# Performance work log

Hardware: AMD Instinct MI355X
Metric: run time of the kernel (lower is better)

Reference implementation:

```python
import jax, jax.numpy as jnp
import numpy as np

DIM = 192
HEADS = 6
HIDDEN = 384  # int(DIM * 2.0)


def _ln(x, w, b):
    # WithBias LayerNorm over channel dim (torch normalizes last dim of b,(hw),c)
    mu = jnp.mean(x, axis=1, keepdims=True)
    var = jnp.var(x, axis=1, keepdims=True)
    return (x - mu) / jnp.sqrt(var + 1e-5) * w[None, :, None, None] + b[None, :, None, None]


def _conv1x1(x, w):  # w: [O, I, 1, 1]
    return jnp.einsum('bihw,oi->bohw', x, w[:, :, 0, 0])


def _dwconv3(x, w):  # depthwise 3x3, w: [C, 1, 3, 3]
    return jax.lax.conv_general_dilated(
        x, w, window_strides=(1, 1), padding=((1, 1), (1, 1)),
        feature_group_count=x.shape[1],
        dimension_numbers=('NCHW', 'OIHW', 'NCHW'))


def _l2norm(x):  # F.normalize along last axis
    n = jnp.sqrt(jnp.sum(x * x, axis=-1, keepdims=True))
    return x / jnp.maximum(n, 1e-12)


def setup_inputs() -> dict:
    key = jax.random.key(0)
    ks = jax.random.split(key, 16)
    s = 0.02
    d = {}
    d['x'] = jax.random.normal(ks[0], (2, DIM, 128, 128), dtype=jnp.float32)
    d['k_v'] = jax.random.normal(ks[1], (2, 256), dtype=jnp.float32)
    d['ln1_w'] = jnp.ones((DIM,), jnp.float32)
    d['ln1_b'] = jnp.zeros((DIM,), jnp.float32)
    d['temp'] = jnp.ones((HEADS, 1, 1), jnp.float32)
    d['w_kR'] = jax.random.normal(ks[2], (DIM * 3 // 4, 192), jnp.float32) * s
    d['w_kI'] = jax.random.normal(ks[3], (DIM // 4, 64), jnp.float32) * s
    d['w_qR'] = jax.random.normal(ks[4], (DIM, DIM * 3 // 4, 1, 1), jnp.float32) * s
    d['w_qdw'] = jax.random.normal(ks[5], (DIM, 1, 3, 3), jnp.float32) * s
    d['w_kvI'] = jax.random.normal(ks[6], (DIM * 2, DIM // 4, 1, 1), jnp.float32) * s
    d['w_kvdw'] = jax.random.normal(ks[7], (DIM * 2, 1, 3, 3), jnp.float32) * s
    d['w_po'] = jax.random.normal(ks[8], (DIM, DIM, 1, 1), jnp.float32) * s
    d['ln2_w'] = jnp.ones((DIM,), jnp.float32)
    d['ln2_b'] = jnp.zeros((DIM,), jnp.float32)
    d['w_ffk'] = jax.random.normal(ks[9], (DIM, 256), jnp.float32) * s
    d['w_pin'] = jax.random.normal(ks[10], (HIDDEN * 2, DIM, 1, 1), jnp.float32) * s
    d['w_dw'] = jax.random.normal(ks[11], (HIDDEN * 2, 1, 3, 3), jnp.float32) * s
    d['w_pout'] = jax.random.normal(ks[12], (DIM, HIDDEN, 1, 1), jnp.float32) * s
    return d


def reference(x, k_v, ln1_w, ln1_b, temp, w_kR, w_kI, w_qR, w_qdw, w_kvI, w_kvdw,
              w_po, ln2_w, ln2_b, w_ffk, w_pin, w_dw, w_pout):
    b, c, h, w = x.shape
    c3 = c * 3 // 4
    # ---- Rttention on norm1(x) ----
    xn = _ln(x, ln1_w, ln1_b)
    kvr = (k_v[:, :192] @ w_kR.T)[:, :, None, None]   # [b, 3c/4, 1, 1]
    kvi = (k_v[:, 192:] @ w_kI.T)[:, :, None, None]   # [b, c/4, 1, 1]
    x_r = xn[:, :c3] * kvr + xn[:, :c3]
    x_i = xn[:, c3:] * kvi + xn[:, c3:]
    q = _dwconv3(_conv1x1(x_r, w_qR), w_qdw)          # [b, c, h, w]
    kv = _dwconv3(_conv1x1(x_i, w_kvI), w_kvdw)       # [b, 2c, h, w]
    k, v = jnp.split(kv, 2, axis=1)
    rh = lambda t: t.reshape(b, HEADS, c // HEADS, h * w)
    q = _l2norm(rh(q))
    k = _l2norm(rh(k))
    v = rh(v)
    # channel-wise attention: [b, head, c_h, c_h]
    attn = jax.nn.softmax(jnp.einsum('bhcd,bhed->bhce', q, k) * temp[None], axis=-1)
    out = jnp.einsum('bhce,bhed->bhcd', attn, v).reshape(b, c, h, w)
    x = x + _conv1x1(out, w_po)
    # ---- GDFN FeedForward on norm2(x) ----
    xn2 = _ln(x, ln2_w, ln2_b)
    kvf = (k_v @ w_ffk.T)[:, :, None, None]           # [b, c, 1, 1]
    y = xn2 * kvf + xn2
    y = _dwconv3(_conv1x1(y, w_pin), w_dw)            # [b, 2*hidden, h, w]
    y1, y2 = jnp.split(y, 2, axis=1)
    y = jax.nn.gelu(y1, approximate=False) * y2
    x = x + _conv1x1(y, w_pout)
    return (x, k_v)
```

## Files before the change

### kernel.cpp

```cpp
#include <hip/hip_runtime.h>
#include <math.h>

#define HW 16384
#define IMG 128
#define CDIM 192
#define C3 144
#define C4 48
#define NB 2
#define NPX 32768
#define HEADS 6

typedef unsigned short u16;
typedef unsigned int u32;
typedef __attribute__((ext_vector_type(8))) short bf16x8;
typedef __attribute__((ext_vector_type(4))) float f32x4;

__device__ __forceinline__ float bf2f(u16 u) {
    return __uint_as_float(((unsigned int)u) << 16);
}
__device__ __forceinline__ u16 f2bf(float f) {
    unsigned int x = __float_as_uint(f);
    unsigned int r = x + 0x7fffu + ((x >> 16) & 1u);
    return (u16)(r >> 16);
}

static inline float* wsf(void* ws, size_t off) { return (float*)((char*)ws + off); }
static inline u16* wsh(void* ws, size_t off) { return (u16*)((char*)ws + off); }

__global__ void k_setup(const float* __restrict__ kvv, const float* __restrict__ wkR,
                        const float* __restrict__ wkI, const float* __restrict__ wffk,
                        const float* __restrict__ wqR, const float* __restrict__ wkvI,
                        const float* __restrict__ wpo, const float* __restrict__ wpin,
                        const float* __restrict__ wpout,
                        u16* __restrict__ wb, float* __restrict__ sm,
                        float* __restrict__ tail) {
    int t = blockIdx.x * 256 + threadIdx.x;
    if (t < 313344) {
        float v;
        if (t < 30720) {
            int o = t / 160, i = t % 160;
            v = (i < 144) ? wqR[o * 144 + i] : 0.f;
        } else if (t < 55296) {
            int r = t - 30720; int o = r / 64, i = r % 64;
            v = (i < 48) ? wkvI[o * 48 + i] : 0.f;
        } else if (t < 92160) {
            v = wpo[t - 55296];
        } else if (t < 239616) {
            v = wpin[t - 92160];
        } else {
            v = wpout[t - 239616];
        }
        wb[t] = f2bf(v);
    } else if (t < 314112) {
        int r = t - 313344;
        if (r < 288) {
            int b = r / 144, o = r % 144;
            const float* v = kvv + b * 256;
            const float* w = wkR + o * 192;
            float s = 0.f;
            for (int j = 0; j < 192; j++) s += v[j] * w[j];
            sm[r] = s + 1.0f;
        } else if (r < 384) {
            int r2 = r - 288;
            int b = r2 / 48, o = r2 % 48;
            const float* v = kvv + b * 256 + 192;
            const float* w = wkI + o * 64;
            float s = 0.f;
            for (int j = 0; j < 64; j++) s += v[j] * w[j];
            sm[288 + r2] = s + 1.0f;
        } else {
            int r2 = r - 384;
            int b = r2 / 192, o = r2 % 192;
            const float* v = kvv + b * 256;
            const float* w = wffk + o * 256;
            float s = 0.f;
            for (int j = 0; j < 256; j++) s += v[j] * w[j];
            sm[384 + r2] = s + 1.0f;
        }
    } else if (t < 314624) {
        int r = t - 314112;
        tail[r] = kvv[r];
    } else if (t < 326912) {
        sm[3840 + (t - 314624)] = 0.f;
    }
}

__global__ void k_setup2(const float* __restrict__ wpin, const float* __restrict__ lnw,
                         const float* __restrict__ lnb, const float* __restrict__ kvf,
                         u16* __restrict__ wpinb, float* __restrict__ rsum,
                         float* __restrict__ biasp) {
    int t = blockIdx.x * 256 + threadIdx.x;
    if (t >= 1536) return;
    int b = t / 768, m = t % 768;
    float rs = 0.f, bi = 0.f;
    u16* wrow = wpinb + (size_t)t * 192;
    for (int c = 0; c < 192; c++) {
        float w = wpin[m * 192 + c];
        float s = kvf[b * 192 + c];
        u16 h = f2bf(w * lnw[c] * s);
        wrow[c] = h;
        rs += bf2f(h);
        bi += w * lnb[c] * s;
    }
    rsum[t] = rs;
    biasp[t] = bi;
}

__global__ __launch_bounds__(256) void k_ln1(
    const float* __restrict__ x,
    const float* __restrict__ lnw, const float* __restrict__ lnb,
    const float* __restrict__ sca, const float* __restrict__ scb,
    u16* __restrict__ outA, u16* __restrict__ outB, u16* __restrict__ xb16) {
    __shared__ float red[2][16][16][4];
    __shared__ float mu_s[16][4], rstd_s[16][4];
    int t = threadIdx.x;
    int px4 = t & 15, cg = t >> 4;
    int base = blockIdx.x * 64;
    int b = base >> 14;
    int p = (base & 16383) + px4 * 4;
    float vals[12][4];
    float s[4] = {0.f, 0.f, 0.f, 0.f}, s2[4] = {0.f, 0.f, 0.f, 0.f};
#pragma unroll
    for (int j = 0; j < 12; j++) {
        int c = cg * 12 + j;
        size_t off = ((size_t)(b * CDIM + c)) * HW + p;
        float4 f = *(const float4*)(x + off);
        float v[4] = {f.x, f.y, f.z, f.w};
        ushort4 o;
        o.x = f2bf(v[0]); o.y = f2bf(v[1]); o.z = f2bf(v[2]); o.w = f2bf(v[3]);
        *(ushort4*)(xb16 + off) = o;
#pragma unroll
        for (int q = 0; q < 4; q++) { vals[j][q] = v[q]; s[q] += v[q]; s2[q] += v[q] * v[q]; }
    }
#pragma unroll
    for (int q = 0; q < 4; q++) { red[0][cg][px4][q] = s[q]; red[1][cg][px4][q] = s2[q]; }
    __syncthreads();
    if (t < 16) {
        float S[4] = {0.f, 0.f, 0.f, 0.f}, S2[4] = {0.f, 0.f, 0.f, 0.f};
        for (int g2 = 0; g2 < 16; g2++)
#pragma unroll
            for (int q = 0; q < 4; q++) { S[q] += red[0][g2][t][q]; S2[q] += red[1][g2][t][q]; }
#pragma unroll
        for (int q = 0; q < 4; q++) {
            float mu = S[q] * (1.0f / CDIM);
            float var = S2[q] * (1.0f / CDIM) - mu * mu;
            mu_s[t][q] = mu;
            rstd_s[t][q] = rsqrtf(var + 1e-5f);
        }
    }
    __syncthreads();
    float mu[4], rs[4];
#pragma unroll
    for (int q = 0; q < 4; q++) { mu[q] = mu_s[px4][q]; rs[q] = rstd_s[px4][q]; }
#pragma unroll
    for (int j = 0; j < 12; j++) {
        int c = cg * 12 + j;
        float w = lnw[c], bb = lnb[c];
        float sc; u16* op; size_t off;
        if (c < C3) { sc = sca[b * C3 + c]; off = ((size_t)(b * C3 + c)) * HW + p; op = outA; }
        else { sc = scb[b * C4 + c - C3]; off = ((size_t)(b * C4 + c - C3)) * HW + p; op = outB; }
        ushort4 o;
        o.x = f2bf(((vals[j][0] - mu[0]) * rs[0] * w + bb) * sc);
        o.y = f2bf(((vals[j][1] - mu[1]) * rs[1] * w + bb) * sc);
        o.z = f2bf(((vals[j][2] - mu[2]) * rs[2] * w + bb) * sc);
        o.w = f2bf(((vals[j][3] - mu[3]) * rs[3] * w + bb) * sc);
        *(ushort4*)(op + off) = o;
    }
}

__global__ __launch_bounds__(256) void k_gemm_qkv(
    const u16* __restrict__ Xq, const u16* __restrict__ Xkv,
    const u16* __restrict__ Wq, const u16* __restrict__ Wkv,
    u16* __restrict__ Oq, u16* __restrict__ Okv) {
    __shared__ __align__(16) u16 Ws[64 * 32];
    __shared__ __align__(16) u16 Xs[32 * 130];
    const int tid = threadIdx.x;
    const int n0 = blockIdx.x * 128;
    const int y = blockIdx.y;
    const int b = blockIdx.z;
    const u16* X; const u16* Wb; u16* Op; int nch, cip, xrows, CO, m0;
    if (y < 3) { X = Xq; Wb = Wq; Op = Oq; nch = 5; cip = 160; xrows = 144; CO = 192; m0 = y * 64; }
    else { X = Xkv; Wb = Wkv; Op = Okv; nch = 2; cip = 64; xrows = 48; CO = 384; m0 = (y - 3) * 64; }
    const u16* Xb = X + (size_t)b * xrows * HW + n0;
    const int wave = tid >> 6, lane = tid & 63;
    const int quad = lane >> 4, l16 = lane & 15;
    const int smr = tid >> 2, sk4 = tid & 3;
    const int skr = tid >> 3, sc0 = (tid & 7) * 16;
    f32x4 acc[4][2] = {};
    for (int ch = 0; ch < nch; ch++) {
        const int k0 = ch * 32;
        if (ch) __syncthreads();
        {
            const int4 wv = *(const int4*)(Wb + (size_t)(m0 + smr) * cip + k0 + sk4 * 8);
            *(int4*)&Ws[(smr << 5) + (((sk4 ^ (smr & 3)) & 3) << 3)] = wv;
        }
        {
            const u16* xc = Xb + (size_t)(k0 + skr) * HW + sc0;
            int4 r0 = *(const int4*)xc;
            int4 r1 = *(const int4*)(xc + 8);
            u32* dst = (u32*)&Xs[skr * 130 + sc0];
#pragma unroll
            for (int i = 0; i < 4; i++) dst[i] = ((const u32*)&r0)[i];
#pragma unroll
            for (int i = 0; i < 4; i++) dst[4 + i] = ((const u32*)&r1)[i];
        }
        __syncthreads();
        bf16x8 af[4];
#pragma unroll
        for (int mi = 0; mi < 4; mi++) {
            int row = mi * 16 + l16;
            af[mi] = *(const bf16x8*)&Ws[(row << 5) + ((quad ^ (row & 3)) << 3)];
        }
#pragma unroll
        for (int ni = 0; ni < 2; ni++) {
            int n = wave * 32 + ni * 16 + l16;
            bf16x8 bfr;
#pragma unroll
            for (int j = 0; j < 8; j++) bfr[j] = (short)Xs[(quad * 8 + j) * 130 + n];
#pragma unroll
            for (int mi = 0; mi < 4; mi++)
                acc[mi][ni] = __builtin_amdgcn_mfma_f32_16x16x32_bf16(af[mi], bfr, acc[mi][ni], 0, 0, 0);
        }
    }
#pragma unroll
    for (int mi = 0; mi < 4; mi++)
#pragma unroll
        for (int ni = 0; ni < 2; ni++)
#pragma unroll
            for (int r = 0; r < 4; r++) {
                int m = m0 + mi * 16 + quad * 4 + r;
                int n = n0 + wave * 32 + ni * 16 + l16;
                Op[((size_t)b * CO + m) * HW + n] = f2bf(acc[mi][ni][r]);
            }
}

__global__ __launch_bounds__(256) void k_dw2m(const u16* __restrict__ Xq,
                                              const u16* __restrict__ Xkv,
                                              const float* __restrict__ Wdq,
                                              const float* __restrict__ Wdkv,
                                              u16* __restrict__ outq, u16* __restrict__ outkv,
                                              float* __restrict__ sqq, float* __restrict__ sqk) {
    __shared__ float In[34 * 132];
    __shared__ float red[4];
    int bid = blockIdx.x;
    const u16* X; const float* Wd; u16* out; float* sqp; int C;
    if (bid < 1536) { X = Xq; Wd = Wdq; out = outq; sqp = sqq; C = 192; }
    else { bid -= 1536; X = Xkv; Wd = Wdkv; out = outkv; sqp = sqk; C = 384; }
    int bc = bid >> 2, rt = bid & 3;
    int b = bc / C, ch = bc % C;
    const u16* xb = X + (size_t)bc * HW;
    int t = threadIdx.x;
    int c0 = (t & 7) * 16;
    for (int r = t >> 3; r < 34; r += 32) {
        int y = rt * 32 - 1 + r;
        float* dst = &In[r * 132 + 1 + c0];
        if ((unsigned)y < 128u) {
            const u16* src = xb + y * 128 + c0;
            int4 r0 = *(const int4*)src;
            int4 r1 = *(const int4*)(src + 8);
            const u16* p0 = (const u16*)&r0;
            const u16* p1 = (const u16*)&r1;
#pragma unroll
            for (int i = 0; i < 8; i++) dst[i] = bf2f(p0[i]);
#pragma unroll
            for (int i = 0; i < 8; i++) dst[8 + i] = bf2f(p1[i]);
        } else {
#pragma unroll
            for (int i = 0; i < 16; i++) dst[i] = 0.f;
        }
    }
    if (t < 34) { In[t * 132] = 0.f; In[t * 132 + 129] = 0.f; }
    __syncthreads();
    const float* w = Wd + ch * 9;
    float w00 = w[0], w01 = w[1], w02 = w[2], w10 = w[3], w11 = w[4],
          w12 = w[5], w20 = w[6], w21 = w[7], w22 = w[8];
    int x = t & 127, rg = t >> 7;
    int base = rg * 16;
    float A2 = 0.f, A1 = 0.f, B1 = 0.f, ssq = 0.f;
    u16* ob = out + (size_t)bc * HW + (rt * 32 + base) * 128 + x;
#pragma unroll
    for (int r = 0; r < 18; r++) {
        const float* row = &In[(base + r) * 132 + x];
        float v0 = row[0], v1 = row[1], v2 = row[2];
        float h0 = w00 * v0 + w01 * v1 + w02 * v2;
        float h1 = w10 * v0 + w11 * v1 + w12 * v2;
        float h2 = w20 * v0 + w21 * v1 + w22 * v2;
        if (r >= 2) {
            float val = A2 + B1 + h2;
            ob[(size_t)(r - 2) * 128] = f2bf(val);
            ssq += val * val;
        }
        A2 = A1; A1 = h0; B1 = h1;
    }
    if (ch < 192) {
        for (int o = 32; o > 0; o >>= 1) ssq += __shfl_down(ssq, o, 64);
        int wid = t >> 6, lane = t & 63;
        if (lane == 0) red[wid] = ssq;
        __syncthreads();
        if (t == 0) sqp[((b * 192 + ch) << 2) | rt] = red[0] + red[1] + red[2] + red[3];
    }
}

__global__ __launch_bounds__(256) void k_qk(const u16* __restrict__ qb_,
                                            const u16* __restrict__ kb_,
                                            float* __restrict__ S) {
    int bh = blockIdx.x >> 5, ds = blockIdx.x & 31;
    int b = bh / HEADS, h = bh % HEADS;
    int tid = threadIdx.x;
    int wave = tid >> 6, lane = tid & 63;
    int quad = lane >> 4, l16 = lane & 15;
    int tm = wave >> 1, tn = wave & 1;
    const u16* qrow = qb_ + ((size_t)(b * 192 + h * 32 + tm * 16 + l16)) * HW + ds * 512 + quad * 8;
    const u16* krow = kb_ + ((size_t)(b * 384 + h * 32 + tn * 16 + l16)) * HW + ds * 512 + quad * 8;
    f32x4 acc = {};
#pragma unroll
    for (int ch = 0; ch < 16; ch++) {
        bf16x8 a = *(const bf16x8*)(qrow + ch * 32);
        bf16x8 k8 = *(const bf16x8*)(krow + ch * 32);
        acc = __builtin_amdgcn_mfma_f32_16x16x32_bf16(a, k8, acc, 0, 0, 0);
    }
    float* Sb = S + bh * 1024;
#pragma unroll
    for (int r = 0; r < 4; r++)
        atomicAdd(&Sb[(tm * 16 + quad * 4 + r) * 32 + tn * 16 + l16], acc[r]);
}

__global__ __launch_bounds__(256) void k_smA(const float* __restrict__ S,
                                             const float* __restrict__ sqqp,
                                             const float* __restrict__ sqkp,
                                             const float* __restrict__ temp,
                                             const float* __restrict__ wpo,
                                             u16* __restrict__ weff) {
    __shared__ float A[32][33];
    __shared__ float scq[32], sck[32];
    int bh = blockIdx.x;
    int b = bh / HEADS, h = bh % HEADS;
    int t = threadIdx.x;
    if (t < 32) {
        const float* qp = sqqp + (b * 192 + h * 32 + t) * 4;
        const float* kp = sqkp + (b * 192 + h * 32 + t) * 4;
        scq[t] = 1.0f / fmaxf(sqrtf(qp[0] + qp[1] + qp[2] + qp[3]), 1e-12f);
        sck[t] = 1.0f / fmaxf(sqrtf(kp[0] + kp[1] + kp[2] + kp[3]), 1e-12f);
    }
    __syncthreads();
    float tmp = temp[h];
    for (int idx = t; idx < 1024; idx += 256) {
        int r = idx >> 5, e = idx & 31;
        A[r][e] = S[bh * 1024 + r * 32 + e] * scq[r] * sck[e] * tmp;
    }
    __syncthreads();
    if (t < 32) {
        float m = -1e30f;
        for (int e = 0; e < 32; e++) m = fmaxf(m, A[t][e]);
        float s = 0.f;
        for (int e = 0; e < 32; e++) { float ev = expf(A[t][e] - m); A[t][e] = ev; s += ev; }
        float inv = 1.0f / s;
        for (int e = 0; e < 32; e++) A[t][e] *= inv;
    }
    __syncthreads();
    for (int idx = t; idx < 6144; idx += 256) {
        int m = idx >> 5, e = idx & 31;
        float s = 0.f;
        const float* wr = wpo + m * 192 + h * 32;
#pragma unroll 8
        for (int c = 0; c < 32; c++) s += wr[c] * A[c][e];
        weff[((size_t)b * 192 + m) * 192 + h * 32 + e] = f2bf(s);
    }
}

__global__ __launch_bounds__(256) void k_gemm_po(
    const u16* __restrict__ kvb, const u16* __restrict__ weff,
    const u16* __restrict__ residb, u16* __restrict__ x1b,
    float* __restrict__ sumP, float* __restrict__ sum2P) {
    __shared__ __align__(16) u16 Ws[64 * 32];
    __shared__ __align__(16) u16 Xs[32 * 130];
    const int tid = threadIdx.x;
    const int n0 = blockIdx.x * 128;
    const int m0 = blockIdx.y * 64;
    const int b = blockIdx.z;
    const u16* Xb = kvb + ((size_t)b * 384 + 192) * HW + n0;
    const u16* Wb = weff + (size_t)b * 192 * 192;
    const int wave = tid >> 6, lane = tid & 63;
    const int quad = lane >> 4, l16 = lane & 15;
    const int smr = tid >> 2, sk4 = tid & 3;
    const int skr = tid >> 3, sc0 = (tid & 7) * 16;
    f32x4 acc[4][2] = {};
    for (int ch = 0; ch < 6; ch++) {
        const int k0 = ch * 32;
        if (ch) __syncthreads();
        {
            const int4 wv = *(const int4*)(Wb + (size_t)(m0 + smr) * 192 + k0 + sk4 * 8);
            *(int4*)&Ws[(smr << 5) + (((sk4 ^ (smr & 3)) & 3) << 3)] = wv;
        }
        {
            const u16* xc = Xb + (size_t)(k0 + skr) * HW + sc0;
            int4 r0 = *(const int4*)xc;
            int4 r1 = *(const int4*)(xc + 8);
            u32* dst = (u32*)&Xs[skr * 130 + sc0];
#pragma unroll
            for (int i = 0; i < 4; i++) dst[i] = ((const u32*)&r0)[i];
#pragma unroll
            for (int i = 0; i < 4; i++) dst[4 + i] = ((const u32*)&r1)[i];
        }
        __syncthreads();
        bf16x8 af[4];
#pragma unroll
        for (int mi = 0; mi < 4; mi++) {
            int row = mi * 16 + l16;
            af[mi] = *(const bf16x8*)&Ws[(row << 5) + ((quad ^ (row & 3)) << 3)];
        }
#pragma unroll
        for (int ni = 0; ni < 2; ni++) {
            int n = wave * 32 + ni * 16 + l16;
            bf16x8 bfr;
#pragma unroll
            for (int j = 0; j < 8; j++) bfr[j] = (short)Xs[(quad * 8 + j) * 130 + n];
#pragma unroll
            for (int mi = 0; mi < 4; mi++)
                acc[mi][ni] = __builtin_amdgcn_mfma_f32_16x16x32_bf16(af[mi], bfr, acc[mi][ni], 0, 0, 0);
        }
    }
#pragma unroll
    for (int ni = 0; ni < 2; ni++) {
        int nl = wave * 32 + ni * 16 + l16;
        float s1 = 0.f, s2 = 0.f;
#pragma unroll
        for (int mi = 0; mi < 4; mi++)
#pragma unroll
            for (int r = 0; r < 4; r++) {
                int m = m0 + mi * 16 + quad * 4 + r;
                size_t idx = ((size_t)(b * 192 + m)) * HW + n0 + nl;
                float v = acc[mi][ni][r] + bf2f(residb[idx]);
                s1 += v; s2 += v * v;
                x1b[idx] = f2bf(v);
            }
        s1 += __shfl_xor(s1, 16, 64); s1 += __shfl_xor(s1, 32, 64);
        s2 += __shfl_xor(s2, 16, 64); s2 += __shfl_xor(s2, 32, 64);
        if (quad == 0) {
            sumP[((size_t)(b * 3 + blockIdx.y)) * HW + n0 + nl] = s1;
            sum2P[((size_t)(b * 3 + blockIdx.y)) * HW + n0 + nl] = s2;
        }
    }
}

__global__ __launch_bounds__(256) void k_pin(
    const u16* __restrict__ X, const u16* __restrict__ wpb,
    const float* __restrict__ rsum, const float* __restrict__ biasp,
    const float* __restrict__ sumP, const float* __restrict__ sum2P,
    u16* __restrict__ out) {
    __shared__ __align__(16) u16 Ws[64 * 32];
    __shared__ __align__(16) u16 Xs[32 * 130];
    const int tid = threadIdx.x;
    const int n0 = blockIdx.x * 128;
    const int m0 = blockIdx.y * 64;
    const int b = blockIdx.z;
    const u16* Xb = X + (size_t)b * 192 * HW + n0;
    const u16* Wb = wpb + (size_t)b * 768 * 192;
    const int wave = tid >> 6, lane = tid & 63;
    const int quad = lane >> 4, l16 = lane & 15;
    const int smr = tid >> 2, sk4 = tid & 3;
    const int skr = tid >> 3, sc0 = (tid & 7) * 16;
    f32x4 acc[4][2] = {};
    for (int ch = 0; ch < 6; ch++) {
        const int k0 = ch * 32;
        if (ch) __syncthreads();
        {
            const int4 wv = *(const int4*)(Wb + (size_t)(m0 + smr) * 192 + k0 + sk4 * 8);
            *(int4*)&Ws[(smr << 5) + (((sk4 ^ (smr & 3)) & 3) << 3)] = wv;
        }
        {
            const u16* xc = Xb + (size_t)(k0 + skr) * HW + sc0;
            int4 r0 = *(const int4*)xc;
            int4 r1 = *(const int4*)(xc + 8);
            u32* dst = (u32*)&Xs[skr * 130 + sc0];
#pragma unroll
            for (int i = 0; i < 4; i++) dst[i] = ((const u32*)&r0)[i];
#pragma unroll
            for (int i = 0; i < 4; i++) dst[4 + i] = ((const u32*)&r1)[i];
        }
        __syncthreads();
        bf16x8 af[4];
#pragma unroll
        for (int mi = 0; mi < 4; mi++) {
            int row = mi * 16 + l16;
            af[mi] = *(const bf16x8*)&Ws[(row << 5) + ((quad ^ (row & 3)) << 3)];
        }
#pragma unroll
        for (int ni = 0; ni < 2; ni++) {
            int n = wave * 32 + ni * 16 + l16;
            bf16x8 bfr;
#pragma unroll
            for (int j = 0; j < 8; j++) bfr[j] = (short)Xs[(quad * 8 + j) * 130 + n];
#pragma unroll
            for (int mi = 0; mi < 4; mi++)
                acc[mi][ni] = __builtin_amdgcn_mfma_f32_16x16x32_bf16(af[mi], bfr, acc[mi][ni], 0, 0, 0);
        }
    }
    float rsv[4][4], biv[4][4];
#pragma unroll
    for (int mi = 0; mi < 4; mi++)
#pragma unroll
        for (int r = 0; r < 4; r++) {
            int m = m0 + mi * 16 + quad * 4 + r;
            rsv[mi][r] = rsum[b * 768 + m];
            biv[mi][r] = biasp[b * 768 + m];
        }
#pragma unroll
    for (int ni = 0; ni < 2; ni++) {
        int n = n0 + wave * 32 + ni * 16 + l16;
        size_t sb = (size_t)b * 3 * HW + n;
        float P = sumP[sb] + sumP[sb + HW] + sumP[sb + 2 * HW];
        float Q = sum2P[sb] + sum2P[sb + HW] + sum2P[sb + 2 * HW];
        float mu = P * (1.0f / 192.0f);
        float var = Q * (1.0f / 192.0f) - mu * mu;
        float rstd = rsqrtf(var + 1e-5f);
#pragma unroll
        for (int mi = 0; mi < 4; mi++)
#pragma unroll
            for (int r = 0; r < 4; r++) {
                int m = m0 + mi * 16 + quad * 4 + r;
                float v = rstd * (acc[mi][ni][r] - mu * rsv[mi][r]) + biv[mi][r];
                out[((size_t)(b * 768 + m)) * HW + n] = f2bf(v);
            }
    }
}

__global__ __launch_bounds__(256) void k_dw_gelu2(const u16* __restrict__ G0,
                                                  const float* __restrict__ Wd,
                                                  u16* __restrict__ out) {
    __shared__ float In[2 * 34 * 132];
    int bc = blockIdx.x >> 2, rt = blockIdx.x & 3;
    int b = bc / 384, j = bc % 384;
    int t = threadIdx.x;
    int c0 = (t & 7) * 16;
    for (int pl = 0; pl < 2; pl++) {
        const u16* xb = G0 + ((size_t)b * 768 + pl * 384 + j) * HW;
        float* pla = &In[pl * 34 * 132];
        for (int r = t >> 3; r < 34; r += 32) {
            int y = rt * 32 - 1 + r;
            float* dst = &pla[r * 132 + 1 + c0];
            if ((unsigned)y < 128u) {
                const u16* src = xb + y * 128 + c0;
                int4 r0 = *(const int4*)src;
                int4 r1 = *(const int4*)(src + 8);
                const u16* p0 = (const u16*)&r0;
                const u16* p1 = (const u16*)&r1;
#pragma unroll
                for (int i = 0; i < 8; i++) dst[i] = bf2f(p0[i]);
#pragma unroll
                for (int i = 0; i < 8; i++) dst[8 + i] = bf2f(p1[i]);
            } else {
#pragma unroll
                for (int i = 0; i < 16; i++) dst[i] = 0.f;
            }
        }
        if (t < 34) { pla[t * 132] = 0.f; pla[t * 132 + 129] = 0.f; }
    }
    __syncthreads();
    const float* w1 = Wd + j * 9;
    const float* w2 = Wd + (384 + j) * 9;
    float a00 = w1[0], a01 = w1[1], a02 = w1[2], a10 = w1[3], a11 = w1[4],
          a12 = w1[5], a20 = w1[6], a21 = w1[7], a22 = w1[8];
    float b00 = w2[0], b01 = w2[1], b02 = w2[2], b10 = w2[3], b11 = w2[4],
          b12 = w2[5], b20 = w2[6], b21 = w2[7], b22 = w2[8];
    int x = t & 127, rg = t >> 7;
    int base = rg * 16;
    float A2a = 0.f, A1a = 0.f, B1a = 0.f;
    float A2b = 0.f, A1b = 0.f, B1b = 0.f;
    u16* ob = out + ((size_t)b * 384 + j) * HW + (rt * 32 + base) * 128 + x;
#pragma unroll
    for (int r = 0; r < 18; r++) {
        const float* r1p = &In[(base + r) * 132 + x];
        const float* r2p = r1p + 34 * 132;
        float u0 = r1p[0], u1 = r1p[1], u2 = r1p[2];
        float v0 = r2p[0], v1 = r2p[1], v2 = r2p[2];
        float h0a = a00 * u0 + a01 * u1 + a02 * u2;
        float h1a = a10 * u0 + a11 * u1 + a12 * u2;
        float h2a = a20 * u0 + a21 * u1 + a22 * u2;
        float h0b = b00 * v0 + b01 * v1 + b02 * v2;
        float h1b = b10 * v0 + b11 * v1 + b12 * v2;
        float h2b = b20 * v0 + b21 * v1 + b22 * v2;
        if (r >= 2) {
            float s1 = A2a + B1a + h2a;
            float s2 = A2b + B1b + h2b;
            float g = 0.5f * s1 * (1.0f + erff(s1 * 0.70710678118654752f));
            ob[(size_t)(r - 2) * 128] = f2bf(g * s2);
        }
        A2a = A1a; A1a = h0a; B1a = h1a;
        A2b = A1b; A1b = h0b; B1b = h1b;
    }
}

__global__ __launch_bounds__(256) void k_gemm_pout(
    const u16* __restrict__ X, const u16* __restrict__ Wb,
    const u16* __restrict__ residb, float* __restrict__ out) {
    __shared__ __align__(16) u16 Ws[64 * 32];
    __shared__ __align__(16) u16 Xs[32 * 130];
    const int tid = threadIdx.x;
    const int n0 = blockIdx.x * 128;
    const int m0 = blockIdx.y * 64;
    const int b = blockIdx.z;
    const u16* Xb = X + (size_t)b * 384 * HW + n0;
    const int wave = tid >> 6, lane = tid & 63;
    const int quad = lane >> 4, l16 = lane & 15;
    const int smr = tid >> 2, sk4 = tid & 3;
    const int skr = tid >> 3, sc0 = (tid & 7) * 16;
    f32x4 acc[4][2] = {};
    for (int ch = 0; ch < 12; ch++) {
        const int k0 = ch * 32;
        if (ch) __syncthreads();
        {
            const int4 wv = *(const int4*)(Wb + (size_t)(m0 + smr) * 384 + k0 + sk4 * 8);
            *(int4*)&Ws[(smr << 5) + (((sk4 ^ (smr & 3)) & 3) << 3)] = wv;
        }
        {
            const u16* xc = Xb + (size_t)(k0 + skr) * HW + sc0;
            int4 r0 = *(const int4*)xc;
            int4 r1 = *(const int4*)(xc + 8);
            u32* dst = (u32*)&Xs[skr * 130 + sc0];
#pragma unroll
            for (int i = 0; i < 4; i++) dst[i] = ((const u32*)&r0)[i];
#pragma unroll
            for (int i = 0; i < 4; i++) dst[4 + i] = ((const u32*)&r1)[i];
        }
        __syncthreads();
        bf16x8 af[4];
#pragma unroll
        for (int mi = 0; mi < 4; mi++) {
            int row = mi * 16 + l16;
            af[mi] = *(const bf16x8*)&Ws[(row << 5) + ((quad ^ (row & 3)) << 3)];
        }
#pragma unroll
        for (int ni = 0; ni < 2; ni++) {
            int n = wave * 32 + ni * 16 + l16;
            bf16x8 bfr;
#pragma unroll
            for (int j = 0; j < 8; j++) bfr[j] = (short)Xs[(quad * 8 + j) * 130 + n];
#pragma unroll
            for (int mi = 0; mi < 4; mi++)
                acc[mi][ni] = __builtin_amdgcn_mfma_f32_16x16x32_bf16(af[mi], bfr, acc[mi][ni], 0, 0, 0);
        }
    }
#pragma unroll
    for (int mi = 0; mi < 4; mi++)
#pragma unroll
        for (int ni = 0; ni < 2; ni++)
#pragma unroll
            for (int r = 0; r < 4; r++) {
                int m = m0 + mi * 16 + quad * 4 + r;
                int n = n0 + wave * 32 + ni * 16 + l16;
                size_t idx = ((size_t)(b * 192 + m)) * HW + n;
                out[idx] = acc[mi][ni][r] + bf2f(residb[idx]);
            }
}

extern "C" void kernel_launch(void* const* d_in, const int* in_sizes, int n_in,
                              void* d_out, int out_size, void* d_ws, size_t ws_size,
                              hipStream_t stream) {
    const float* x     = (const float*)d_in[0];
    const float* k_v   = (const float*)d_in[1];
    const float* ln1w  = (const float*)d_in[2];
    const float* ln1b  = (const float*)d_in[3];
    const float* temp  = (const float*)d_in[4];
    const float* w_kR  = (const float*)d_in[5];
    const float* w_kI  = (const float*)d_in[6];
    const float* w_qR  = (const float*)d_in[7];
    const float* w_qdw = (const float*)d_in[8];
    const float* w_kvI = (const float*)d_in[9];
    const float* w_kvdw= (const float*)d_in[10];
    const float* w_po  = (const float*)d_in[11];
    const float* ln2w  = (const float*)d_in[12];
    const float* ln2b  = (const float*)d_in[13];
    const float* w_ffk = (const float*)d_in[14];
    const float* w_pin = (const float*)d_in[15];
    const float* w_dw  = (const float*)d_in[16];
    const float* w_pout= (const float*)d_in[17];
    float* out = (float*)d_out;

    const size_t MiB = 1048576ULL;
    u16*   xrb     = wsh(d_ws, 0);
    u16*   xib     = wsh(d_ws, 10 * MiB);
    u16*   xb16    = wsh(d_ws, 14 * MiB);
    u16*   q0b     = wsh(d_ws, 26 * MiB);
    u16*   kv0b    = wsh(d_ws, 38 * MiB);
    u16*   qbuf_b  = wsh(d_ws, 62 * MiB);
    u16*   kvbuf_b = wsh(d_ws, 74 * MiB);
    u16*   x1b     = wsh(d_ws, 98 * MiB);
    u16*   g0b     = wsh(d_ws, 110 * MiB);
    u16*   ybufb   = wsh(d_ws, 158 * MiB);
    u16*   wb      = wsh(d_ws, 182 * MiB);
    u16*   weffb   = wsh(d_ws, 183 * MiB);
    u16*   wpinb   = wsh(d_ws, 184 * MiB);
    float* sm      = wsf(d_ws, 185 * MiB);
    float* sumP    = wsf(d_ws, 186 * MiB);
    float* sum2P   = wsf(d_ws, 187 * MiB);
    u16* wq   = wb;
    u16* wkv  = wb + 30720;
    u16* wpout= wb + 239616;
    float* kvr  = sm;
    float* kvi  = sm + 288;
    float* kvf  = sm + 384;
    float* sqqp = sm + 768;
    float* sqkp = sm + 2304;
    float* Smat = sm + 3840;
    float* rsum = sm + 16128;
    float* biasp= sm + 17664;

    k_setup<<<1277, 256, 0, stream>>>(k_v, w_kR, w_kI, w_ffk, w_qR, w_kvI, w_po,
                                      w_pin, w_pout, wb, sm,
                                      out + (size_t)NB * CDIM * HW);
    k_setup2<<<6, 256, 0, stream>>>(w_pin, ln2w, ln2b, kvf, wpinb, rsum, biasp);
    k_ln1<<<NPX / 64, 256, 0, stream>>>(x, ln1w, ln1b, kvr, kvi, xrb, xib, xb16);
    k_gemm_qkv<<<dim3(128, 9, 2), 256, 0, stream>>>(xrb, xib, wq, wkv, q0b, kv0b);
    k_dw2m<<<4608, 256, 0, stream>>>(q0b, kv0b, w_qdw, w_kvdw, qbuf_b, kvbuf_b, sqqp, sqkp);
    k_qk<<<12 * 32, 256, 0, stream>>>(qbuf_b, kvbuf_b, Smat);
    k_smA<<<12, 256, 0, stream>>>(Smat, sqqp, sqkp, temp, w_po, weffb);
    k_gemm_po<<<dim3(128, 3, 2), 256, 0, stream>>>(kvbuf_b, weffb, xb16, x1b, sumP, sum2P);
    k_pin<<<dim3(128, 12, 2), 256, 0, stream>>>(x1b, wpinb, rsum, biasp, sumP, sum2P, g0b);
    k_dw_gelu2<<<NB * 384 * 4, 256, 0, stream>>>(g0b, w_dw, ybufb);
    k_gemm_pout<<<dim3(128, 3, 2), 256, 0, stream>>>(ybufb, wpout, x1b, out);
}
```

Before: 280.6 us.

## Merge setup kernels and keep depthwise conv halos in bf16 shared memory

```diff
diff --git a/kernel.cpp b/kernel.cpp
--- a/kernel.cpp
+++ b/kernel.cpp
@@ -30,80 +30,83 @@
 __global__ void k_setup(const float* __restrict__ kvv, const float* __restrict__ wkR,
                         const float* __restrict__ wkI, const float* __restrict__ wffk,
                         const float* __restrict__ wqR, const float* __restrict__ wkvI,
-                        const float* __restrict__ wpo, const float* __restrict__ wpin,
-                        const float* __restrict__ wpout,
+                        const float* __restrict__ wpout_f, const float* __restrict__ wpin,
+                        const float* __restrict__ ln2w, const float* __restrict__ ln2b,
                         u16* __restrict__ wb, float* __restrict__ sm,
-                        float* __restrict__ tail) {
-    int t = blockIdx.x * 256 + threadIdx.x;
-    if (t < 313344) {
-        float v;
-        if (t < 30720) {
-            int o = t / 160, i = t % 160;
-            v = (i < 144) ? wqR[o * 144 + i] : 0.f;
-        } else if (t < 55296) {
-            int r = t - 30720; int o = r / 64, i = r % 64;
-            v = (i < 48) ? wkvI[o * 48 + i] : 0.f;
-        } else if (t < 92160) {
-            v = wpo[t - 55296];
-        } else if (t < 239616) {
-            v = wpin[t - 92160];
-        } else {
-            v = wpout[t - 239616];
-        }
-        wb[t] = f2bf(v);
-    } else if (t < 314112) {
-        int r = t - 313344;
-        if (r < 288) {
-            int b = r / 144, o = r % 144;
-            const float* v = kvv + b * 256;
-            const float* w = wkR + o * 192;
-            float s = 0.f;
-            for (int j = 0; j < 192; j++) s += v[j] * w[j];
-            sm[r] = s + 1.0f;
-        } else if (r < 384) {
-            int r2 = r - 288;
-            int b = r2 / 48, o = r2 % 48;
-            const float* v = kvv + b * 256 + 192;
-            const float* w = wkI + o * 64;
-            float s = 0.f;
-            for (int j = 0; j < 64; j++) s += v[j] * w[j];
-            sm[288 + r2] = s + 1.0f;
-        } else {
-            int r2 = r - 384;
-            int b = r2 / 192, o = r2 % 192;
+                        u16* __restrict__ wpinb, float* __restrict__ rsum,
+                        float* __restrict__ biasp, float* __restrict__ tail) {
+    int blk = blockIdx.x;
+    if (blk < 460) {
+        int t = blk * 256 + threadIdx.x;
+        if (t < 104448) {
+            float v;
+            if (t < 30720) {
+                int o = t / 160, i = t % 160;
+                v = (i < 144) ? wqR[o * 144 + i] : 0.f;
+            } else if (t < 55296) {
+                int r = t - 30720; int o = r / 64, i = r % 64;
+                v = (i < 48) ? wkvI[o * 48 + i] : 0.f;
+            } else {
+                v = wpout_f[t - 55296];
+            }
+            wb[t] = f2bf(v);
+        } else if (t < 104832) {
+            int r = t - 104448;
+            if (r < 288) {
+                int b = r / 144, o = r % 144;
+                const float* v = kvv + b * 256;
+                const float* w = wkR + o * 192;
+                float s = 0.f;
+                for (int j = 0; j < 192; j++) s += v[j] * w[j];
+                sm[r] = s + 1.0f;
+            } else {
+                int r2 = r - 288;
+                int b = r2 / 48, o = r2 % 48;
+                const float* v = kvv + b * 256 + 192;
+                const float* w = wkI + o * 64;
+                float s = 0.f;
+                for (int j = 0; j < 64; j++) s += v[j] * w[j];
+                sm[288 + r2] = s + 1.0f;
+            }
+        } else if (t < 105344) {
+            tail[t - 104832] = kvv[t - 104832];
+        } else if (t < 117632) {
+            sm[3840 + (t - 105344)] = 0.f;
+        }
+    } else {
+        __shared__ float kvfl[384];
+        int wid = threadIdx.x >> 6, lane = threadIdx.x & 63;
+        for (int r = wid; r < 384; r += 4) {
+            int b = r / 192, o = r % 192;
             const float* v = kvv + b * 256;
             const float* w = wffk + o * 256;
             float s = 0.f;
-            for (int j = 0; j < 256; j++) s += v[j] * w[j];
-            sm[384 + r2] = s + 1.0f;
-        }
-    } else if (t < 314624) {
-        int r = t - 314112;
-        tail[r] = kvv[r];
-    } else if (t < 326912) {
-        sm[3840 + (t - 314624)] = 0.f;
-    }
-}
-
-__global__ void k_setup2(const float* __restrict__ wpin, const float* __restrict__ lnw,
-                         const float* __restrict__ lnb, const float* __restrict__ kvf,
-                         u16* __restrict__ wpinb, float* __restrict__ rsum,
-                         float* __restrict__ biasp) {
-    int t = blockIdx.x * 256 + threadIdx.x;
-    if (t >= 1536) return;
-    int b = t / 768, m = t % 768;
-    float rs = 0.f, bi = 0.f;
-    u16* wrow = wpinb + (size_t)t * 192;
-    for (int c = 0; c < 192; c++) {
-        float w = wpin[m * 192 + c];
-        float s = kvf[b * 192 + c];
-        u16 h = f2bf(w * lnw[c] * s);
-        wrow[c] = h;
-        rs += bf2f(h);
-        bi += w * lnb[c] * s;
-    }
-    rsum[t] = rs;
-    biasp[t] = bi;
+            for (int j = lane; j < 256; j += 64) s += v[j] * w[j];
+            for (int o2 = 32; o2 > 0; o2 >>= 1) s += __shfl_down(s, o2, 64);
+            if (lane == 0) kvfl[r] = s + 1.0f;
+        }
+        __syncthreads();
+        int row = (blk - 460) * 4 + wid;
+        int b = row / 768, m = row % 768;
+        const float* wr = wpin + m * 192;
+        u16* wrow = wpinb + (size_t)row * 192;
+        float rs = 0.f, bi = 0.f;
+#pragma unroll
+        for (int j = 0; j < 3; j++) {
+            int c = lane + j * 64;
+            float w = wr[c];
+            float s = kvfl[b * 192 + c];
+            u16 h = f2bf(w * ln2w[c] * s);
+            wrow[c] = h;
+            rs += bf2f(h);
+            bi += w * ln2b[c] * s;
+        }
+        for (int o2 = 32; o2 > 0; o2 >>= 1) {
+            rs += __shfl_down(rs, o2, 64);
+            bi += __shfl_down(bi, o2, 64);
+        }
+        if (lane == 0) { rsum[row] = rs; biasp[row] = bi; }
+    }
 }
 
 __global__ __launch_bounds__(256) void k_ln1(
@@ -240,8 +243,8 @@
                                               const float* __restrict__ Wdkv,
                                               u16* __restrict__ outq, u16* __restrict__ outkv,
                                               float* __restrict__ sqq, float* __restrict__ sqk) {
-    __shared__ float In[34 * 132];
-    __shared__ float red[4];
+    __shared__ __align__(16) u16 In[34 * 144];
+    __shared__ float redf[4];
     int bid = blockIdx.x;
     const u16* X; const float* Wd; u16* out; float* sqp; int C;
     if (bid < 1536) { X = Xq; Wd = Wdq; out = outq; sqp = sqq; C = 192; }
@@ -253,23 +256,16 @@
     int c0 = (t & 7) * 16;
     for (int r = t >> 3; r < 34; r += 32) {
         int y = rt * 32 - 1 + r;
-        float* dst = &In[r * 132 + 1 + c0];
+        u16* dst = In + r * 144 + 8 + c0;
         if ((unsigned)y < 128u) {
-            const u16* src = xb + y * 128 + c0;
-            int4 r0 = *(const int4*)src;
-            int4 r1 = *(const int4*)(src + 8);
-            const u16* p0 = (const u16*)&r0;
-            const u16* p1 = (const u16*)&r1;
-#pragma unroll
-            for (int i = 0; i < 8; i++) dst[i] = bf2f(p0[i]);
-#pragma unroll
-            for (int i = 0; i < 8; i++) dst[8 + i] = bf2f(p1[i]);
+            const int4* s4 = (const int4*)(xb + y * 128 + c0);
+            ((int4*)dst)[0] = s4[0]; ((int4*)dst)[1] = s4[1];
         } else {
-#pragma unroll
-            for (int i = 0; i < 16; i++) dst[i] = 0.f;
-        }
-    }
-    if (t < 34) { In[t * 132] = 0.f; In[t * 132 + 129] = 0.f; }
+            int4 z = make_int4(0, 0, 0, 0);
+            ((int4*)dst)[0] = z; ((int4*)dst)[1] = z;
+        }
+    }
+    if (t < 34) { In[t * 144 + 7] = 0; In[t * 144 + 136] = 0; }
     __syncthreads();
     const float* w = Wd + ch * 9;
     float w00 = w[0], w01 = w[1], w02 = w[2], w10 = w[3], w11 = w[4],
@@ -280,8 +276,8 @@
     u16* ob = out + (size_t)bc * HW + (rt * 32 + base) * 128 + x;
 #pragma unroll
     for (int r = 0; r < 18; r++) {
-        const float* row = &In[(base + r) * 132 + x];
-        float v0 = row[0], v1 = row[1], v2 = row[2];
+        const u16* row = In + (base + r) * 144 + 8 + x;
+        float v0 = bf2f(row[-1]), v1 = bf2f(row[0]), v2 = bf2f(row[1]);
         float h0 = w00 * v0 + w01 * v1 + w02 * v2;
         float h1 = w10 * v0 + w11 * v1 + w12 * v2;
         float h2 = w20 * v0 + w21 * v1 + w22 * v2;
@@ -295,9 +291,9 @@
     if (ch < 192) {
         for (int o = 32; o > 0; o >>= 1) ssq += __shfl_down(ssq, o, 64);
         int wid = t >> 6, lane = t & 63;
-        if (lane == 0) red[wid] = ssq;
+        if (lane == 0) redf[wid] = ssq;
         __syncthreads();
-        if (t == 0) sqp[((b * 192 + ch) << 2) | rt] = red[0] + red[1] + red[2] + red[3];
+        if (t == 0) sqp[((b * 192 + ch) << 2) | rt] = redf[0] + redf[1] + redf[2] + redf[3];
     }
 }
 
@@ -528,33 +524,26 @@
 __global__ __launch_bounds__(256) void k_dw_gelu2(const u16* __restrict__ G0,
                                                   const float* __restrict__ Wd,
                                                   u16* __restrict__ out) {
-    __shared__ float In[2 * 34 * 132];
+    __shared__ __align__(16) u16 In2[2 * 34 * 144];
     int bc = blockIdx.x >> 2, rt = blockIdx.x & 3;
     int b = bc / 384, j = bc % 384;
     int t = threadIdx.x;
     int c0 = (t & 7) * 16;
     for (int pl = 0; pl < 2; pl++) {
         const u16* xb = G0 + ((size_t)b * 768 + pl * 384 + j) * HW;
-        float* pla = &In[pl * 34 * 132];
+        u16* pla = In2 + pl * 34 * 144;
         for (int r = t >> 3; r < 34; r += 32) {
             int y = rt * 32 - 1 + r;
-            float* dst = &pla[r * 132 + 1 + c0];
+            u16* dst = pla + r * 144 + 8 + c0;
             if ((unsigned)y < 128u) {
-                const u16* src = xb + y * 128 + c0;
-                int4 r0 = *(const int4*)src;
-                int4 r1 = *(const int4*)(src + 8);
-                const u16* p0 = (const u16*)&r0;
-                const u16* p1 = (const u16*)&r1;
-#pragma unroll
-                for (int i = 0; i < 8; i++) dst[i] = bf2f(p0[i]);
-#pragma unroll
-                for (int i = 0; i < 8; i++) dst[8 + i] = bf2f(p1[i]);
+                const int4* s4 = (const int4*)(xb + y * 128 + c0);
+                ((int4*)dst)[0] = s4[0]; ((int4*)dst)[1] = s4[1];
             } else {
-#pragma unroll
-                for (int i = 0; i < 16; i++) dst[i] = 0.f;
+                int4 z = make_int4(0, 0, 0, 0);
+                ((int4*)dst)[0] = z; ((int4*)dst)[1] = z;
             }
         }
-        if (t < 34) { pla[t * 132] = 0.f; pla[t * 132 + 129] = 0.f; }
+        if (t < 34) { pla[t * 144 + 7] = 0; pla[t * 144 + 136] = 0; }
     }
     __syncthreads();
     const float* w1 = Wd + j * 9;
@@ -570,10 +559,10 @@
     u16* ob = out + ((size_t)b * 384 + j) * HW + (rt * 32 + base) * 128 + x;
 #pragma unroll
     for (int r = 0; r < 18; r++) {
-        const float* r1p = &In[(base + r) * 132 + x];
-        const float* r2p = r1p + 34 * 132;
-        float u0 = r1p[0], u1 = r1p[1], u2 = r1p[2];
-        float v0 = r2p[0], v1 = r2p[1], v2 = r2p[2];
+        const u16* r1p = In2 + (base + r) * 144 + 8 + x;
+        const u16* r2p = r1p + 34 * 144;
+        float u0 = bf2f(r1p[-1]), u1 = bf2f(r1p[0]), u2 = bf2f(r1p[1]);
+        float v0 = bf2f(r2p[-1]), v1 = bf2f(r2p[0]), v2 = bf2f(r2p[1]);
         float h0a = a00 * u0 + a01 * u1 + a02 * u2;
         float h1a = a10 * u0 + a11 * u1 + a12 * u2;
         float h2a = a20 * u0 + a21 * u1 + a22 * u2;
@@ -696,20 +685,19 @@
     float* sum2P   = wsf(d_ws, 187 * MiB);
     u16* wq   = wb;
     u16* wkv  = wb + 30720;
-    u16* wpout= wb + 239616;
+    u16* wpout= wb + 55296;
     float* kvr  = sm;
     float* kvi  = sm + 288;
-    float* kvf  = sm + 384;
     float* sqqp = sm + 768;
     float* sqkp = sm + 2304;
     float* Smat = sm + 3840;
     float* rsum = sm + 16128;
     float* biasp= sm + 17664;
 
-    k_setup<<<1277, 256, 0, stream>>>(k_v, w_kR, w_kI, w_ffk, w_qR, w_kvI, w_po,
-                                      w_pin, w_pout, wb, sm,
-                                      out + (size_t)NB * CDIM * HW);
-    k_setup2<<<6, 256, 0, stream>>>(w_pin, ln2w, ln2b, kvf, wpinb, rsum, biasp);
+    k_setup<<<844, 256, 0, stream>>>(k_v, w_kR, w_kI, w_ffk, w_qR, w_kvI,
+                                     w_pout, w_pin, ln2w, ln2b,
+                                     wb, sm, wpinb, rsum, biasp,
+                                     out + (size_t)NB * CDIM * HW);
     k_ln1<<<NPX / 64, 256, 0, stream>>>(x, ln1w, ln1b, kvr, kvi, xrb, xib, xb16);
     k_gemm_qkv<<<dim3(128, 9, 2), 256, 0, stream>>>(xrb, xib, wq, wkv, q0b, kv0b);
     k_dw2m<<<4608, 256, 0, stream>>>(q0b, kv0b, w_qdw, w_kvdw, qbuf_b, kvbuf_b, sqqp, sqkp);
```

New measurement: 381.7 us. +36.0%, slower.
